# Optimization experiments

Hardware: AMD Instinct MI355X
Metric: run time of the kernel (lower is better)

Reference implementation:

```python
import jax, jax.numpy as jnp
import numpy as np

B, S = 4096, 8192


def setup_inputs() -> dict:
    key = jax.random.key(0)
    k1, k2 = jax.random.split(key)
    input_attenuation = jax.random.normal(k1, (B, S), dtype=jnp.float32)
    input_wet_dry = jax.random.randint(k2, (B, S), 0, 2, dtype=jnp.int32)
    return {"input_attenuation": input_attenuation, "input_wet_dry": input_wet_dry}


def reference(input_attenuation, input_wet_dry):
    # Forward-fill: baseline[n] = attenuation at the most recent index m <= n
    # with wet_dry[m] == 0 (index 0 always counts, matching baseline[0] = A[0]).
    # Expressed as a parallel cummax over candidate indices + gather.
    _, S_ = input_attenuation.shape
    idx = jnp.arange(S_, dtype=jnp.int32)
    valid = (input_wet_dry == 0) | (idx[None, :] == 0)  # [B,S]
    cand = jnp.where(valid, idx[None, :], jnp.int32(-1))
    src = jax.lax.cummax(cand, axis=1)  # last dry index so far, always >= 0
    return jnp.take_along_axis(input_attenuation, src, axis=1)
```

## Files before the change

kernel.cpp:

```cpp
#include <hip/hip_runtime.h>


typedef float f32x4 __attribute__((ext_vector_type(4)));
typedef int i32x4 __attribute__((ext_vector_type(4)));

constexpr int S_CONST = 8192;
constexpr int CHUNK = 512;
constexpr int NCHUNK = S_CONST / CHUNK;

__global__ __launch_bounds__(256) void ffill_kernel(const float* __restrict__ A,
                                                    const int* __restrict__ W,
                                                    float* __restrict__ O,
                                                    int B) {
    const int wave = (blockIdx.x * blockDim.x + threadIdx.x) >> 6;
    const int lane = threadIdx.x & 63;
    if (wave >= B) return;

    const f32x4* __restrict__ Arow =
        reinterpret_cast<const f32x4*>(A + (size_t)wave * S_CONST);
    const i32x4* __restrict__ Wrow =
        reinterpret_cast<const i32x4*>(W + (size_t)wave * S_CONST);
    f32x4* __restrict__ Orow =
        reinterpret_cast<f32x4*>(O + (size_t)wave * S_CONST);

    float carry = 0.0f;
    const unsigned long long below = ((unsigned long long)1 << lane) - 1ull;

    #pragma unroll 4
    for (int c = 0; c < NCHUNK; ++c) {
        const int base = c * 128 + lane;
        const f32x4 a1 = Arow[base];
        const f32x4 a2 = Arow[base + 64];
        const i32x4 w1 = Wrow[base];
        const i32x4 w2 = Wrow[base + 64];

        const bool first = (c == 0) & (lane == 0);

        float v1 = 0.f; int d1 = 0;
        if ((w1.x == 0) | first) { v1 = a1.x; d1 = 1; }
        if (w1.y == 0)           { v1 = a1.y; d1 = 1; }
        if (w1.z == 0)           { v1 = a1.z; d1 = 1; }
        if (w1.w == 0)           { v1 = a1.w; d1 = 1; }
        float v2 = 0.f; int d2 = 0;
        if (w2.x == 0) { v2 = a2.x; d2 = 1; }
        if (w2.y == 0) { v2 = a2.y; d2 = 1; }
        if (w2.z == 0) { v2 = a2.z; d2 = 1; }
        if (w2.w == 0) { v2 = a2.w; d2 = 1; }

        const unsigned long long m1 = __ballot(d1);
        const unsigned long long m2 = __ballot(d2);
        const unsigned long long p1 = m1 & below;
        const unsigned long long p2 = m2 & below;

        const int src1 = 63 - __clzll(p1 | 1ull);
        const int src2 = 63 - __clzll(p2 | 1ull);
        const int top1 = 63 - __clzll(m1 | 1ull);
        const int top2 = 63 - __clzll(m2 | 1ull);

        const float f1 = __shfl(v1, src1);
        const float g1 = __shfl(v1, top1);
        const float f2 = __shfl(v2, src2);
        const float g2 = __shfl(v2, top2);

        const float fillA = m1 ? g1 : carry;
        const float seed1 = p1 ? f1 : carry;
        const float seed2 = p2 ? f2 : fillA;
        carry = m2 ? g2 : fillA;

        f32x4 o;
        float run = seed1;
        if ((w1.x == 0) | first) run = a1.x;
        o.x = run;
        if (w1.y == 0) run = a1.y;
        o.y = run;
        if (w1.z == 0) run = a1.z;
        o.z = run;
        if (w1.w == 0) run = a1.w;
        o.w = run;
        __builtin_nontemporal_store(o, &Orow[base]);

        run = seed2;
        if (w2.x == 0) run = a2.x;
        o.x = run;
        if (w2.y == 0) run = a2.y;
        o.y = run;
        if (w2.z == 0) run = a2.z;
        o.z = run;
        if (w2.w == 0) run = a2.w;
        o.w = run;
        __builtin_nontemporal_store(o, &Orow[base + 64]);
    }
}

extern "C" void kernel_launch(void* const* d_in, const int* in_sizes, int n_in,
                              void* d_out, int out_size, void* d_ws, size_t ws_size,
                              hipStream_t stream) {
    const float* A = (const float*)d_in[0];
    const int* W = (const int*)d_in[1];
    float* O = (float*)d_out;

    const int B = in_sizes[0] / S_CONST;

    const int threads = 256;
    const int blocks = (B * 64 + threads - 1) / threads;
    hipLaunchKernelGGL(ffill_kernel, dim3(blocks), dim3(threads), 0, stream,
                       A, W, O, B);
}
```

Before: 63.27 us.

## Split each row across four waves with shared-memory carry propagation

Each block now handles one row, with four waves each processing a quarter segment. Every wave preloads all its chunks into registers, computes its local last-dry value, and publishes it via shared memory. After a barrier, each wave seeds its forward-fill from the preceding segments. This aims to expose more memory-level parallelism than the serial per-wave chunk loop, at the cost of higher register use and a block-wide sync.

```diff
diff --git a/kernel.cpp b/kernel.cpp
--- a/kernel.cpp
+++ b/kernel.cpp
@@ -5,90 +5,131 @@
 typedef int i32x4 __attribute__((ext_vector_type(4)));
 
 constexpr int S_CONST = 8192;
-constexpr int CHUNK = 512;
-constexpr int NCHUNK = S_CONST / CHUNK;
+constexpr int NWAVE = 4;
+constexpr int SEG = S_CONST / NWAVE;
+constexpr int NC = SEG / 512;
 
 __global__ __launch_bounds__(256) void ffill_kernel(const float* __restrict__ A,
                                                     const int* __restrict__ W,
                                                     float* __restrict__ O,
                                                     int B) {
-    const int wave = (blockIdx.x * blockDim.x + threadIdx.x) >> 6;
+    const int row = blockIdx.x;
+    const int wid = threadIdx.x >> 6;
     const int lane = threadIdx.x & 63;
-    if (wave >= B) return;
 
-    const f32x4* __restrict__ Arow =
-        reinterpret_cast<const f32x4*>(A + (size_t)wave * S_CONST);
-    const i32x4* __restrict__ Wrow =
-        reinterpret_cast<const i32x4*>(W + (size_t)wave * S_CONST);
-    f32x4* __restrict__ Orow =
-        reinterpret_cast<f32x4*>(O + (size_t)wave * S_CONST);
+    __shared__ float s_val[NWAVE];
+    __shared__ int s_has[NWAVE];
 
-    float carry = 0.0f;
+    const size_t seg_off = (size_t)row * (S_CONST / 4) + wid * (SEG / 4);
+    const f32x4* __restrict__ Aseg = reinterpret_cast<const f32x4*>(A) + seg_off;
+    const i32x4* __restrict__ Wseg = reinterpret_cast<const i32x4*>(W) + seg_off;
+    f32x4* __restrict__ Oseg = reinterpret_cast<f32x4*>(O) + seg_off;
+
     const unsigned long long below = ((unsigned long long)1 << lane) - 1ull;
 
-    #pragma unroll 4
-    for (int c = 0; c < NCHUNK; ++c) {
+    f32x4 a1[NC], a2[NC];
+    float f1[NC], f2[NC], g1[NC], g2[NC];
+    int dm[NC];
+    unsigned long long m1s[NC], m2s[NC];
+
+    float segval = 0.0f;
+    int seghas = 0;
+
+    #pragma unroll
+    for (int c = 0; c < NC; ++c) {
         const int base = c * 128 + lane;
-        const f32x4 a1 = Arow[base];
-        const f32x4 a2 = Arow[base + 64];
-        const i32x4 w1 = Wrow[base];
-        const i32x4 w2 = Wrow[base + 64];
+        a1[c] = Aseg[base];
+        a2[c] = Aseg[base + 64];
+        const i32x4 w1 = Wseg[base];
+        const i32x4 w2 = Wseg[base + 64];
 
-        const bool first = (c == 0) & (lane == 0);
+        const bool first = (wid == 0) & (c == 0) & (lane == 0);
 
-        float v1 = 0.f; int d1 = 0;
-        if ((w1.x == 0) | first) { v1 = a1.x; d1 = 1; }
-        if (w1.y == 0)           { v1 = a1.y; d1 = 1; }
-        if (w1.z == 0)           { v1 = a1.z; d1 = 1; }
-        if (w1.w == 0)           { v1 = a1.w; d1 = 1; }
-        float v2 = 0.f; int d2 = 0;
-        if (w2.x == 0) { v2 = a2.x; d2 = 1; }
-        if (w2.y == 0) { v2 = a2.y; d2 = 1; }
-        if (w2.z == 0) { v2 = a2.z; d2 = 1; }
-        if (w2.w == 0) { v2 = a2.w; d2 = 1; }
+        int d = 0;
+        if ((w1.x == 0) | first) d |= 1;
+        if (w1.y == 0) d |= 2;
+        if (w1.z == 0) d |= 4;
+        if (w1.w == 0) d |= 8;
+        if (w2.x == 0) d |= 16;
+        if (w2.y == 0) d |= 32;
+        if (w2.z == 0) d |= 64;
+        if (w2.w == 0) d |= 128;
+        dm[c] = d;
 
-        const unsigned long long m1 = __ballot(d1);
-        const unsigned long long m2 = __ballot(d2);
+        float v1 = 0.f;
+        if (d & 1) v1 = a1[c].x;
+        if (d & 2) v1 = a1[c].y;
+        if (d & 4) v1 = a1[c].z;
+        if (d & 8) v1 = a1[c].w;
+        float v2 = 0.f;
+        if (d & 16) v2 = a2[c].x;
+        if (d & 32) v2 = a2[c].y;
+        if (d & 64) v2 = a2[c].z;
+        if (d & 128) v2 = a2[c].w;
+
+        const unsigned long long m1 = __ballot((d & 15) != 0);
+        const unsigned long long m2 = __ballot((d >> 4) != 0);
+        m1s[c] = m1;
+        m2s[c] = m2;
+
         const unsigned long long p1 = m1 & below;
         const unsigned long long p2 = m2 & below;
+        f1[c] = __shfl(v1, 63 - __clzll(p1 | 1ull));
+        g1[c] = __shfl(v1, 63 - __clzll(m1 | 1ull));
+        f2[c] = __shfl(v2, 63 - __clzll(p2 | 1ull));
+        g2[c] = __shfl(v2, 63 - __clzll(m2 | 1ull));
 
-        const int src1 = 63 - __clzll(p1 | 1ull);
-        const int src2 = 63 - __clzll(p2 | 1ull);
-        const int top1 = 63 - __clzll(m1 | 1ull);
-        const int top2 = 63 - __clzll(m2 | 1ull);
+        if (m1) segval = g1[c];
+        if (m2) segval = g2[c];
+        seghas |= (m1 | m2) != 0ull;
+    }
 
-        const float f1 = __shfl(v1, src1);
-        const float g1 = __shfl(v1, top1);
-        const float f2 = __shfl(v2, src2);
-        const float g2 = __shfl(v2, top2);
+    if (lane == 0) {
+        s_val[wid] = segval;
+        s_has[wid] = seghas;
+    }
+    __syncthreads();
 
-        const float fillA = m1 ? g1 : carry;
-        const float seed1 = p1 ? f1 : carry;
-        const float seed2 = p2 ? f2 : fillA;
-        carry = m2 ? g2 : fillA;
+    float seed = 0.0f;
+    for (int j = wid - 1; j >= 0; --j) {
+        if (s_has[j]) { seed = s_val[j]; break; }
+    }
 
+    float carry = seed;
+    #pragma unroll
+    for (int c = 0; c < NC; ++c) {
+        const int base = c * 128 + lane;
+        const unsigned long long p1 = m1s[c] & below;
+        const unsigned long long p2 = m2s[c] & below;
+
+        const float fillA = (m1s[c] != 0ull) ? g1[c] : carry;
+        const float seed1 = p1 ? f1[c] : carry;
+        const float seed2 = p2 ? f2[c] : fillA;
+        carry = (m2s[c] != 0ull) ? g2[c] : fillA;
+
+        const int d = dm[c];
         f32x4 o;
         float run = seed1;
-        if ((w1.x == 0) | first) run = a1.x;
+        if (d & 1) run = a1[c].x;
         o.x = run;
-        if (w1.y == 0) run = a1.y;
+        if (d & 2) run = a1[c].y;
         o.y = run;
-        if (w1.z == 0) run = a1.z;
+        if (d & 4) run = a1[c].z;
         o.z = run;
-        if (w1.w == 0) run = a1.w;
+        if (d & 8) run = a1[c].w;
         o.w = run;
-        __builtin_nontemporal_store(o, &Orow[base]);
+        __builtin_nontemporal_store(o, &Oseg[base]);
 
         run = seed2;
-        if (w2.x == 0) run = a2.x;
+        if (d & 16) run = a2[c].x;
         o.x = run;
-        if (w2.y == 0) run = a2.y;
+        if (d & 32) run = a2[c].y;
         o.y = run;
-        if (w2.z == 0) run = a2.z;
+        if (d & 64) run = a2[c].z;
         o.z = run;
-        if (w2.w == 0) run = a2.w;
+        if (d & 128) run = a2[c].w;
         o.w = run;
-        __builtin_nontemporal_store(o, &Orow[base + 64]);
+        __builtin_nontemporal_store(o, &Oseg[base + 64]);
     }
 }
 
@@ -101,8 +142,5 @@
 
     const int B = in_sizes[0] / S_CONST;
 
-    const int threads = 256;
-    const int blocks = (B * 64 + threads - 1) / threads;
-    hipLaunchKernelGGL(ffill_kernel, dim3(blocks), dim3(threads), 0, stream,
-                       A, W, O, B);
+    hipLaunchKernelGGL(ffill_kernel, dim3(B), dim3(256), 0, stream, A, W, O, B);
 }
```

After: 61.92 us. 2.1% less time.
